# Kernel optimization log

Hardware: AMD Instinct MI355X
Metric: run time of the kernel (lower is better)

The kernel has to match this reference:

```python
import jax, jax.numpy as jnp
import numpy as np

B, H, L = 16, 512, 2048
N2 = 32  # d_state/2 complex modes
DT_MIN, DT_MAX = 1e-3, 1e-1


def setup_inputs() -> dict:
    key = jax.random.key(0)
    ks = jax.random.split(key, 8)
    u = jax.random.normal(ks[0], (B, H, L), dtype=jnp.float32)
    D = jax.random.normal(ks[1], (H,), dtype=jnp.float32)
    # log-uniform timescales in [DT_MIN, DT_MAX]
    r = jax.random.uniform(ks[2], (H,), dtype=jnp.float32)
    log_dt = (np.log(DT_MIN) + r * (np.log(DT_MAX) - np.log(DT_MIN))).astype(jnp.float32)
    C_re = jax.random.normal(ks[3], (H, N2), dtype=jnp.float32)
    C_im = jax.random.normal(ks[4], (H, N2), dtype=jnp.float32)
    W1 = jax.random.normal(ks[5], (L, 2 * H), dtype=jnp.float32) / np.float32(np.sqrt(L))
    b1 = jnp.zeros((2 * H,), dtype=jnp.float32)
    W2 = jax.random.normal(ks[6], (2 * H, H), dtype=jnp.float32) / np.float32(np.sqrt(2 * H))
    b2 = jnp.zeros((H,), dtype=jnp.float32)
    return {"u": u, "D": D, "log_dt": log_dt, "C_re": C_re, "C_im": C_im,
            "W1": W1, "b1": b1, "W2": W2, "b2": b2}


def _s4d_kernel(log_dt, C_re, C_im, length):
    # S4D-Lin: A_n = -1/2 + i*pi*n
    n = jnp.arange(N2, dtype=jnp.float32)
    A = -0.5 + 1j * jnp.pi * n                      # (N2,)
    dt = jnp.exp(log_dt)                             # (H,)
    dtA = dt[:, None] * A[None, :]                   # (H, N2)
    C = (C_re + 1j * C_im) * (jnp.exp(dtA) - 1.0) / A
    # Vandermonde: k[h, l] = 2 * Re sum_n C[h,n] * exp(dtA[h,n] * l)
    K = jnp.exp(dtA[:, :, None] * jnp.arange(length, dtype=jnp.float32))  # (H, N2, L)
    return 2.0 * jnp.einsum('hn,hnl->hl', C, K).real  # (H, L)


def reference(u, D, log_dt, C_re, C_im, W1, b1, W2, b2):
    # u: (B, H, L)
    k = _s4d_kernel(log_dt, C_re, C_im, L)           # (H, L)
    k_f = jnp.fft.rfft(k, n=2 * L, axis=-1)          # (H, L+1)
    u_f = jnp.fft.rfft(u, n=2 * L, axis=-1)          # (B, H, L+1)
    y = jnp.fft.irfft(u_f * k_f[None], n=2 * L, axis=-1)[..., :L]
    y = y + u * D[:, None]
    y = jax.nn.gelu(y, approximate=False)
    # keras Conv1D(k=1) / tanh / Dense applied to channels-first tensor:
    # dense over last axis L -> 2H, tanh, dense 2H -> H
    y = jnp.tanh(jnp.einsum('bhl,lf->bhf', y, W1) + b1)  # (B, H, 2H)
    y = jnp.einsum('bhf,fo->bho', y, W2) + b2            # (B, H, H)
    return y
```

## Files before the change

### kernel.cpp

```cpp
#include <hip/hip_runtime.h>
#include <math.h>

#define B_  16
#define H_  512
#define L_  2048
#define N2_ 32
#define NC_ 16
#define LC_ 128

typedef __attribute__((ext_vector_type(8))) short short8;
typedef __attribute__((ext_vector_type(4))) float f32x4;

__device__ __forceinline__ short f2bf(float x) {
    unsigned u = __builtin_bit_cast(unsigned, x);
    u += 0x7fffu + ((u >> 16) & 1u);
    return (short)(u >> 16);
}
__device__ __forceinline__ float bf2f(unsigned short s) {
    unsigned u = ((unsigned)s) << 16;
    return __builtin_bit_cast(float, u);
}

__global__ void k0_table(const float* __restrict__ log_dt,
                         const float* __restrict__ C_re,
                         const float* __restrict__ C_im,
                         float4* __restrict__ tab) {
    int idx = blockIdx.x * blockDim.x + threadIdx.x;
    if (idx >= H_ * N2_) return;
    int h = idx >> 5, n = idx & 31;
    float dt = expf(log_dt[h]);
    float e  = expf(-0.5f * dt);
    float th = 3.14159265358979323846f * (float)n * dt;
    float lr = e * cosf(th), li = e * sinf(th);
    float ar = -0.5f, ai = 3.14159265358979323846f * (float)n;
    float den = ar * ar + ai * ai;
    float x = lr - 1.0f, y = li;
    float nr = (x * ar + y * ai) / den;
    float ni = (y * ar - x * ai) / den;
    float cr = C_re[idx], ci = C_im[idx];
    tab[idx] = make_float4(lr, li, cr * nr - ci * ni, cr * ni + ci * nr);
}

__global__ void t0_pow(const float4* __restrict__ tab, float2* __restrict__ POW) {
    int t = blockIdx.x * 256 + threadIdx.x;
    if (t >= H_ * N2_) return;
    int h = t >> 5;
    float4 v = tab[t];
    float lr = v.x, li = v.y;
    float pr = 1.0f, pi = 0.0f;
    float2* base = POW + (size_t)h * 129 * N2_ + (t & 31);
    for (int m = 0; m <= 128; ++m) {
        base[(size_t)m * N2_] = make_float2(pr, pi);
        float npr = pr * lr - pi * li;
        float npi = pr * li + pi * lr;
        pr = npr; pi = npi;
    }
}

__global__ void t_ktab(const float4* __restrict__ tab, const float2* __restrict__ POW,
                       const float* __restrict__ Dv, float* __restrict__ ktab) {
    int t = blockIdx.x * 256 + threadIdx.x;
    if (t >= H_ * 128) return;
    int h = t >> 7, m = t & 127;
    const float2* P = POW + (size_t)h * 129 * N2_ + (size_t)m * N2_;
    const float4* tb = tab + h * N2_;
    float s = 0.0f;
    for (int n = 0; n < N2_; ++n) {
        float2 p = P[n];
        float4 v = tb[n];
        s += v.z * p.x - v.w * p.y;
    }
    ktab[t] = 2.0f * s + (m == 0 ? Dv[h] : 0.0f);
}

__global__ void __launch_bounds__(256)
t1_fill(const float4* __restrict__ tab, const float2* __restrict__ POW,
        const float* __restrict__ ktab, short* __restrict__ Psw,
        short* __restrict__ Vsw) {
    int t = blockIdx.x * 256 + threadIdx.x;
    int sub = t & 7;
    int rowg = t >> 3;
    int h = rowg / 320, row = rowg % 320;
    if (row < 192) {
        short8 s0, s1;
        if (row < 128) {
            int l = row;
#pragma unroll
            for (int mm = 0; mm < 8; ++mm) {
                int m0 = sub * 16 + mm, m1 = m0 + 8;
                s0[mm] = (m0 <= l) ? f2bf(ktab[h * 128 + (l - m0)]) : (short)0;
                s1[mm] = (m1 <= l) ? f2bf(ktab[h * 128 + (l - m1)]) : (short)0;
            }
        } else {
            int j = row - 128, nn = j >> 1, part = j & 1;
            const float2* P = POW + (size_t)h * 129 * N2_ + nn;
#pragma unroll
            for (int mm = 0; mm < 8; ++mm) {
                int m0 = sub * 16 + mm, m1 = m0 + 8;
                float2 p0 = P[(size_t)(127 - m0) * N2_];
                float2 p1 = P[(size_t)(127 - m1) * N2_];
                s0[mm] = f2bf(part ? p0.y : p0.x);
                s1[mm] = f2bf(part ? p1.y : p1.x);
            }
        }
        *(short8*)(Psw + ((size_t)(h * 16 + sub * 2 + 0) * 192 + row) * 8) = s0;
        *(short8*)(Psw + ((size_t)(h * 16 + sub * 2 + 1) * 192 + row) * 8) = s1;
    } else {
        int l = row - 192;
        const float2* P = POW + (size_t)h * 129 * N2_ + (size_t)(l + 1) * N2_;
        const float4* tb = tab + h * N2_;
        short8 s;
#pragma unroll
        for (int jj = 0; jj < 8; ++jj) {
            int j = sub * 8 + jj, nn = j >> 1;
            float2 p = P[nn];
            float4 cv = tb[nn];
            float re = cv.z * p.x - cv.w * p.y;
            float im = cv.z * p.y + cv.w * p.x;
            s[jj] = f2bf((j & 1) ? -2.0f * im : 2.0f * re);
        }
        *(short8*)(Vsw + ((size_t)(h * 8 + sub) * 128 + l) * 8) = s;
    }
}

__global__ void __launch_bounds__(512)
conv_mfma(const float* __restrict__ u, const short* __restrict__ Psw,
          float* __restrict__ E, short* __restrict__ Ybuf) {
    __shared__ char smem[65536];
    short* Ps = (short*)smem;
    short* As = (short*)(smem + 49152);
    short* Ys = (short*)smem;
    int h = blockIdx.x;
    int tid = threadIdx.x;
    {
        const short8* Pg = (const short8*)(Psw + (size_t)h * 24576);
        short8* PsV = (short8*)Ps;
#pragma unroll
        for (int j = 0; j < 6; ++j) PsV[tid + j * 512] = Pg[tid + j * 512];
    }
    int row = tid >> 1, half = tid & 1;
    int b0 = row >> 4, c0 = row & 15;
    const float* up = u + ((size_t)(b0 * H_ + h)) * L_ + (size_t)c0 * LC_ + half * 16;
    short8* AsV = (short8*)As;

    int lane = tid & 63, wave = tid >> 6;
    int wm = wave >> 1, wn = wave & 1;
    int lrow = lane & 15, lk = lane >> 4;
    const short8* AsF = (const short8*)As;
    const short8* PsF = (const short8*)Ps;

    f32x4 acc[4][6] = {};
    float4 fv0 = *(const float4*)(up + 0);
    float4 fv1 = *(const float4*)(up + 4);
    float4 fv2 = *(const float4*)(up + 8);
    float4 fv3 = *(const float4*)(up + 12);
    for (int ks = 0; ks < 4; ++ks) {
        __syncthreads();
        short8 s0, s1;
        s0[0] = f2bf(fv0.x); s0[1] = f2bf(fv0.y); s0[2] = f2bf(fv0.z); s0[3] = f2bf(fv0.w);
        s0[4] = f2bf(fv1.x); s0[5] = f2bf(fv1.y); s0[6] = f2bf(fv1.z); s0[7] = f2bf(fv1.w);
        s1[0] = f2bf(fv2.x); s1[1] = f2bf(fv2.y); s1[2] = f2bf(fv2.z); s1[3] = f2bf(fv2.w);
        s1[4] = f2bf(fv3.x); s1[5] = f2bf(fv3.y); s1[6] = f2bf(fv3.z); s1[7] = f2bf(fv3.w);
        AsV[(half * 2 + 0) * 256 + row] = s0;
        AsV[(half * 2 + 1) * 256 + row] = s1;
        __syncthreads();
        if (ks < 3) {
            const float* nx = up + (ks + 1) * 32;
            fv0 = *(const float4*)(nx + 0);
            fv1 = *(const float4*)(nx + 4);
            fv2 = *(const float4*)(nx + 8);
            fv3 = *(const float4*)(nx + 12);
        }
        short8 af[4], bfr[6];
#pragma unroll
        for (int m = 0; m < 4; ++m)
            af[m] = AsF[lk * 256 + wm * 64 + m * 16 + lrow];
#pragma unroll
        for (int n = 0; n < 6; ++n)
            bfr[n] = PsF[(ks * 4 + lk) * 192 + wn * 96 + n * 16 + lrow];
#pragma unroll
        for (int m = 0; m < 4; ++m)
#pragma unroll
            for (int n = 0; n < 6; ++n)
                acc[m][n] = __builtin_amdgcn_mfma_f32_16x16x32_bf16(
                    af[m], bfr[n], acc[m][n], 0, 0, 0);
    }
    __syncthreads();

#pragma unroll
    for (int nf = 0; nf < 6; ++nf) {
        int col = wn * 96 + nf * 16 + lrow;
#pragma unroll
        for (int mf = 0; mf < 4; ++mf) {
            int rb = wm * 64 + mf * 16 + lk * 4;
#pragma unroll
            for (int r = 0; r < 4; ++r) {
                int Rr = rb + r;
                float vv = acc[mf][nf][r];
                if (col < 128) {
                    Ys[Rr * 128 + col] = f2bf(vv);
                } else {
                    int bb = Rr >> 4, cc = Rr & 15;
                    E[((size_t)(bb * H_ + h) * NC_ + cc) * 64 + (col - 128)] = vv;
                }
            }
        }
    }
    __syncthreads();

    const short8* YsV = (const short8*)Ys;
#pragma unroll
    for (int it = 0; it < 8; ++it) {
        int sidx = it * 512 + tid;
        int rr = sidx >> 4;
        int colq = sidx & 15;
        int bb = rr >> 4, cc = rr & 15;
        *(short8*)(Ybuf + ((size_t)(bb * H_ + h)) * L_ + (size_t)cc * LC_ + colq * 8)
            = YsV[sidx];
    }
}

__global__ void k2_scan(const float* __restrict__ log_dt, float2* __restrict__ ES) {
    int t = blockIdx.x * 256 + threadIdx.x;
    if (t >= B_ * H_ * N2_) return;
    int n  = t & 31;
    int h  = (t >> 5) & (H_ - 1);
    int bh = t >> 5;
    float dt = expf(log_dt[h]);
    float e  = expf(-0.5f * dt * (float)LC_);
    float th = 3.14159265358979323846f * (float)n * dt * (float)LC_;
    float Lr = e * cosf(th), Li = e * sinf(th);
    float cr = 0.0f, ci = 0.0f;
    float2* base = ES + (size_t)bh * NC_ * N2_ + n;
#pragma unroll
    for (int c = 0; c < NC_; ++c) {
        float2 Ev = base[(size_t)c * N2_];
        base[(size_t)c * N2_] = make_float2(cr, ci);
        float ncr = fmaf(Lr, cr, fmaf(-Li, ci, Ev.x));
        float nci = fmaf(Lr, ci, fmaf(Li, cr, Ev.y));
        cr = ncr; ci = nci;
    }
}

__global__ void __launch_bounds__(256)
dcarry_mfma(const float* __restrict__ ES, const short* __restrict__ Vsw,
            const short* __restrict__ Ybuf, short* __restrict__ gbf) {
    __shared__ char smem[32768];
    short* Sa = (short*)smem;
    short* Vb = (short*)(smem + 16384);
    short* Ys = (short*)smem;
    int h = blockIdx.x, mh = blockIdx.y;
    int tid = threadIdx.x;
    {
        const short8* Vg = (const short8*)(Vsw + (size_t)h * 8192);
        short8* VbV = (short8*)Vb;
#pragma unroll
        for (int j = 0; j < 4; ++j) VbV[tid + j * 256] = Vg[tid + j * 256];
    }
    int row = tid >> 1, half = tid & 1;
    int R = mh * 128 + row, b = R >> 4, c = R & 15;
    {
        const float* sp = ES + ((size_t)(b * H_ + h) * NC_ + c) * 64 + half * 32;
        short8* SaV = (short8*)Sa;
#pragma unroll
        for (int gg = 0; gg < 4; ++gg) {
            float4 f0 = *(const float4*)(sp + gg * 8);
            float4 f1 = *(const float4*)(sp + gg * 8 + 4);
            short8 s;
            s[0] = f2bf(f0.x); s[1] = f2bf(f0.y); s[2] = f2bf(f0.z); s[3] = f2bf(f0.w);
            s[4] = f2bf(f1.x); s[5] = f2bf(f1.y); s[6] = f2bf(f1.z); s[7] = f2bf(f1.w);
            SaV[(half * 4 + gg) * 128 + row] = s;
        }
    }
    __syncthreads();
    int lane = tid & 63, wave = tid >> 6;
    int wm = wave >> 1, wn = wave & 1;
    int lrow = lane & 15, lk = lane >> 4;
    const short8* SaF = (const short8*)Sa;
    const short8* VbF = (const short8*)Vb;
    f32x4 acc[4][4] = {};
#pragma unroll
    for (int ks = 0; ks < 2; ++ks) {
        int g = ks * 4 + lk;
        short8 af[4], bf[4];
#pragma unroll
        for (int m = 0; m < 4; ++m)
            af[m] = SaF[g * 128 + wm * 64 + m * 16 + lrow];
#pragma unroll
        for (int n = 0; n < 4; ++n)
            bf[n] = VbF[g * 128 + wn * 64 + n * 16 + lrow];
#pragma unroll
        for (int m = 0; m < 4; ++m)
#pragma unroll
            for (int n = 0; n < 4; ++n)
                acc[m][n] = __builtin_amdgcn_mfma_f32_16x16x32_bf16(
                    af[m], bf[n], acc[m][n], 0, 0, 0);
    }
    __syncthreads();

#pragma unroll
    for (int nf = 0; nf < 4; ++nf) {
        int l = wn * 64 + nf * 16 + lrow;
#pragma unroll
        for (int mf = 0; mf < 4; ++mf) {
            int rb = wm * 64 + mf * 16 + lk * 4;
#pragma unroll
            for (int r = 0; r < 4; ++r)
                Ys[(rb + r) * 128 + l] = f2bf(acc[mf][nf][r]);
        }
    }
    __syncthreads();

    const short8* YsV = (const short8*)Ys;
#pragma unroll
    for (int it = 0; it < 8; ++it) {
        int sidx = it * 256 + tid;
        int rr = sidx >> 4;
        int colq = sidx & 15;
        int Rr = mh * 128 + rr, bb = Rr >> 4, cc = Rr & 15;
        size_t gaddr = ((size_t)(bb * H_ + h)) * L_ + (size_t)cc * LC_ + colq * 8;
        short8 yv = *(const short8*)(Ybuf + gaddr);
        short8 cv = YsV[sidx];
        short8 o;
#pragma unroll
        for (int j = 0; j < 8; ++j) {
            float y = bf2f((unsigned short)yv[j]) + bf2f((unsigned short)cv[j]);
            o[j] = f2bf(0.5f * y * (1.0f + erff(y * 0.70710678118654752f)));
        }
        *(short8*)(gbf + gaddr) = o;
    }
}

__global__ void __launch_bounds__(256)
wtrans(const float* __restrict__ W, short* __restrict__ Wt, int K, int N) {
    __shared__ short tile[32][33];
    int bk = blockIdx.x * 32, bn = blockIdx.y * 32;
    int tx = threadIdx.x & 31, ty = threadIdx.x >> 5;
#pragma unroll
    for (int i = 0; i < 4; ++i)
        tile[ty + i * 8][tx] = f2bf(W[(size_t)(bk + ty + i * 8) * N + bn + tx]);
    __syncthreads();
#pragma unroll
    for (int i = 0; i < 4; ++i)
        Wt[(size_t)(bn + ty + i * 8) * K + bk + tx] = tile[tx][ty + i * 8];
}

template<bool TANH, bool OUTBF>
__global__ void __launch_bounds__(512)
gemm_mfma(const short* __restrict__ A, const short* __restrict__ Bt,
          const float* __restrict__ bias, void* __restrict__ Cout,
          int M, int N, int K) {
    __shared__ short As[2][128 * 36];
    __shared__ short Bs[2][128 * 36];
    int tid  = threadIdx.x;
    int lane = tid & 63;
    int wave = tid >> 6;
    int wm = wave >> 2, wn = wave & 3;
    int lrow = lane & 15, kblk = lane >> 4;
    int row0 = blockIdx.x * 128, col0 = blockIdx.y * 128;

    int srow = tid >> 2;
    int sk   = (tid & 3) * 8;
    const short* Ag = A  + (size_t)(row0 + srow) * K + sk;
    const short* Bg = Bt + (size_t)(col0 + srow) * K + sk;
    int si = srow * 36 + sk;

    f32x4 acc[4][2] = {};
    const int NT = K >> 5;

    short8 pa = *(const short8*)(Ag),      pb = *(const short8*)(Bg);
    *(short8*)&As[0][si] = pa;
    *(short8*)&Bs[0][si] = pb;
    short8 qa = *(const short8*)(Ag + 32), qb = *(const short8*)(Bg + 32);
    __syncthreads();

    for (int t = 0; t < NT; t += 2) {
        if (t + 2 < NT) {
            int ko = (t + 2) << 5;
            pa = *(const short8*)(Ag + ko);
            pb = *(const short8*)(Bg + ko);
        }
        {
            short8 af[4], bf[2];
#pragma unroll
            for (int m = 0; m < 4; ++m)
                af[m] = *(const short8*)&As[0][(wm * 64 + m * 16 + lrow) * 36 + kblk * 8];
#pragma unroll
            for (int n = 0; n < 2; ++n)
                bf[n] = *(const short8*)&Bs[0][(wn * 32 + n * 16 + lrow) * 36 + kblk * 8];
#pragma unroll
            for (int m = 0; m < 4; ++m)
#pragma unroll
                for (int n = 0; n < 2; ++n)
                    acc[m][n] = __builtin_amdgcn_mfma_f32_16x16x32_bf16(
                        af[m], bf[n], acc[m][n], 0, 0, 0);
        }
        *(short8*)&As[1][si] = qa;
        *(short8*)&Bs[1][si] = qb;
        __syncthreads();

        if (t + 3 < NT) {
            int ko = (t + 3) << 5;
            qa = *(const short8*)(Ag + ko);
            qb = *(const short8*)(Bg + ko);
        }
        {
            short8 af[4], bf[2];
#pragma unroll
            for (int m = 0; m < 4; ++m)
                af[m] = *(const short8*)&As[1][(wm * 64 + m * 16 + lrow) * 36 + kblk * 8];
#pragma unroll
            for (int n = 0; n < 2; ++n)
                bf[n] = *(const short8*)&Bs[1][(wn * 32 + n * 16 + lrow) * 36 + kblk * 8];
#pragma unroll
            for (int m = 0; m < 4; ++m)
#pragma unroll
                for (int n = 0; n < 2; ++n)
                    acc[m][n] = __builtin_amdgcn_mfma_f32_16x16x32_bf16(
                        af[m], bf[n], acc[m][n], 0, 0, 0);
        }
        if (t + 2 < NT) {
            *(short8*)&As[0][si] = pa;
            *(short8*)&Bs[0][si] = pb;
        }
        __syncthreads();
    }

#pragma unroll
    for (int n = 0; n < 2; ++n) {
        int col = col0 + wn * 32 + n * 16 + lrow;
        float bb = bias[col];
#pragma unroll
        for (int m = 0; m < 4; ++m) {
            int rowb = row0 + wm * 64 + m * 16 + kblk * 4;
#pragma unroll
            for (int r = 0; r < 4; ++r) {
                float v = acc[m][n][r] + bb;
                if (TANH) v = tanhf(v);
                if (OUTBF) ((short*)Cout)[(size_t)(rowb + r) * N + col] = f2bf(v);
                else       ((float*)Cout)[(size_t)(rowb + r) * N + col] = v;
            }
        }
    }
}

extern "C" void kernel_launch(void* const* d_in, const int* in_sizes, int n_in,
                              void* d_out, int out_size, void* d_ws, size_t ws_size,
                              hipStream_t stream) {
    const float* u     = (const float*)d_in[0];
    const float* D     = (const float*)d_in[1];
    const float* logdt = (const float*)d_in[2];
    const float* C_re  = (const float*)d_in[3];
    const float* C_im  = (const float*)d_in[4];
    const float* W1    = (const float*)d_in[5];
    const float* b1    = (const float*)d_in[6];
    const float* W2    = (const float*)d_in[7];
    const float* b2    = (const float*)d_in[8];
    float* out = (float*)d_out;

    char* p = (char*)d_ws;
    float4* tab = (float4*)p;            p += 262144;
    char* regionA = p;                   p += 33554432;
    float2* POW  = (float2*)regionA;
    float*  ktab = (float*)(regionA + 16908288);
    short*  Ybuf = (short*)regionA;
    short* Psw = (short*)p;              p += 25165824;
    short* Vsw = (short*)p;              p += 8388608;
    float* E   = (float*)p;              p += 33554432;
    short* gbf = (short*)p;              p += 33554432;
    short* tb  = (short*)p;              p += 16777216;
    short* w1t = (short*)p;              p += 4194304;
    short* w2t = (short*)p;

    k0_table<<<H_ * N2_ / 256, 256, 0, stream>>>(logdt, C_re, C_im, tab);
    t0_pow  <<<H_ * N2_ / 256, 256, 0, stream>>>(tab, POW);
    t_ktab  <<<H_ * 128 / 256, 256, 0, stream>>>(tab, POW, D, ktab);
    t1_fill <<<H_ * 320 * 8 / 256, 256, 0, stream>>>(tab, POW, ktab, Psw, Vsw);
    wtrans  <<<dim3(L_ / 32, 2 * H_ / 32), 256, 0, stream>>>(W1, w1t, L_, 2 * H_);
    wtrans  <<<dim3(2 * H_ / 32, H_ / 32), 256, 0, stream>>>(W2, w2t, 2 * H_, H_);

    conv_mfma  <<<H_, 512, 0, stream>>>(u, Psw, E, Ybuf);
    k2_scan    <<<B_ * H_ * N2_ / 256, 256, 0, stream>>>(logdt, (float2*)E);
    dcarry_mfma<<<dim3(H_, 2), 256, 0, stream>>>(E, Vsw, Ybuf, gbf);

    gemm_mfma<true, true ><<<dim3(B_ * H_ / 128, 2 * H_ / 128), 512, 0, stream>>>(
        gbf, w1t, b1, tb, B_ * H_, 2 * H_, L_);
    gemm_mfma<false, false><<<dim3(B_ * H_ / 128, H_ / 128), 512, 0, stream>>>(
        tb, w2t, b2, out, B_ * H_, H_, 2 * H_);
}
```

Before: 190.8 us.

## Parallelize power table over all entries and raise MFMA wave priority in GEMM

The power-table kernel previously used one thread per (h,n) and ran a serial 129-step complex multiply chain with strided stores. It now launches one thread per table entry and computes each power directly with exp, cos and sin, which exposes far more parallelism and gives coalesced writes. Separately, the GEMM inner loop wraps its MFMA bursts in s_setprio(1)/s_setprio(0) to favour waves that are issuing matrix instructions. Evaluating the closed form directly changes rounding slightly compared with the repeated multiply, and it adds transcendental calls per entry.

```diff
diff --git a/kernel.cpp b/kernel.cpp
--- a/kernel.cpp
+++ b/kernel.cpp
@@ -41,20 +41,18 @@
     tab[idx] = make_float4(lr, li, cr * nr - ci * ni, cr * ni + ci * nr);
 }
 
-__global__ void t0_pow(const float4* __restrict__ tab, float2* __restrict__ POW) {
+__global__ void __launch_bounds__(256)
+t0_pow(const float* __restrict__ log_dt, float2* __restrict__ POW) {
     int t = blockIdx.x * 256 + threadIdx.x;
-    if (t >= H_ * N2_) return;
-    int h = t >> 5;
-    float4 v = tab[t];
-    float lr = v.x, li = v.y;
-    float pr = 1.0f, pi = 0.0f;
-    float2* base = POW + (size_t)h * 129 * N2_ + (t & 31);
-    for (int m = 0; m <= 128; ++m) {
-        base[(size_t)m * N2_] = make_float2(pr, pi);
-        float npr = pr * lr - pi * li;
-        float npi = pr * li + pi * lr;
-        pr = npr; pi = npi;
-    }
+    if (t >= H_ * 129 * N2_) return;
+    int n = t & 31;
+    int m = (t >> 5) % 129;
+    int h = t / (129 * N2_);
+    float dt = expf(log_dt[h]);
+    float fm = (float)m;
+    float e  = expf(-0.5f * dt * fm);
+    float th = 3.14159265358979323846f * (float)n * dt * fm;
+    POW[t] = make_float2(e * cosf(th), e * sinf(th));
 }
 
 __global__ void t_ktab(const float4* __restrict__ tab, const float2* __restrict__ POW,
@@ -388,12 +386,14 @@
 #pragma unroll
             for (int n = 0; n < 2; ++n)
                 bf[n] = *(const short8*)&Bs[0][(wn * 32 + n * 16 + lrow) * 36 + kblk * 8];
+            __builtin_amdgcn_s_setprio(1);
 #pragma unroll
             for (int m = 0; m < 4; ++m)
 #pragma unroll
                 for (int n = 0; n < 2; ++n)
                     acc[m][n] = __builtin_amdgcn_mfma_f32_16x16x32_bf16(
                         af[m], bf[n], acc[m][n], 0, 0, 0);
+            __builtin_amdgcn_s_setprio(0);
         }
         *(short8*)&As[1][si] = qa;
         *(short8*)&Bs[1][si] = qb;
@@ -412,12 +412,14 @@
 #pragma unroll
             for (int n = 0; n < 2; ++n)
                 bf[n] = *(const short8*)&Bs[1][(wn * 32 + n * 16 + lrow) * 36 + kblk * 8];
+            __builtin_amdgcn_s_setprio(1);
 #pragma unroll
             for (int m = 0; m < 4; ++m)
 #pragma unroll
                 for (int n = 0; n < 2; ++n)
                     acc[m][n] = __builtin_amdgcn_mfma_f32_16x16x32_bf16(
                         af[m], bf[n], acc[m][n], 0, 0, 0);
+            __builtin_amdgcn_s_setprio(0);
         }
         if (t + 2 < NT) {
             *(short8*)&As[0][si] = pa;
@@ -473,7 +475,7 @@
     short* w2t = (short*)p;
 
     k0_table<<<H_ * N2_ / 256, 256, 0, stream>>>(logdt, C_re, C_im, tab);
-    t0_pow  <<<H_ * N2_ / 256, 256, 0, stream>>>(tab, POW);
+    t0_pow  <<<H_ * 129 * N2_ / 256, 256, 0, stream>>>(logdt, POW);
     t_ktab  <<<H_ * 128 / 256, 256, 0, stream>>>(tab, POW, D, ktab);
     t1_fill <<<H_ * 320 * 8 / 256, 256, 0, stream>>>(tab, POW, ktab, Psw, Vsw);
     wtrans  <<<dim3(L_ / 32, 2 * H_ / 32), 256, 0, stream>>>(W1, w1t, L_, 2 * H_);
```

Result: no change. 188.9 us (-1.0%).
